# Performance work log

Hardware: AMD Instinct MI355X
Metric: run time of the kernel (lower is better)

The kernel has to match this reference:

```python
import jax, jax.numpy as jnp
import numpy as np

NUM_HEADS = 32


def setup_inputs() -> dict:
    key = jax.random.key(0)
    ks = jax.random.split(key, 6)
    B, S, E = 1, 2048, 2560
    return {
        "hidden_states": jax.random.normal(ks[0], (B, S, E), dtype=jnp.float32),
        "attention_mask": jnp.zeros((B, 1, 1, S), dtype=jnp.float32),
        "position_bias": jax.random.normal(ks[1], (NUM_HEADS, S, S), dtype=jnp.float32),
        "c_attn_w": jax.random.normal(ks[2], (E, 3 * E), dtype=jnp.float32) * 0.02,
        "c_attn_b": jax.random.normal(ks[3], (3 * E,), dtype=jnp.float32) * 0.02,
        "c_proj_w": jax.random.normal(ks[4], (E, E), dtype=jnp.float32) * 0.02,
        "c_proj_b": jax.random.normal(ks[5], (E,), dtype=jnp.float32) * 0.02,
    }


def reference(hidden_states, attention_mask, position_bias, c_attn_w, c_attn_b, c_proj_w, c_proj_b):
    B, S, E = hidden_states.shape
    H = NUM_HEADS
    D = E // H  # head_dim = 80

    # Fused QKV projection (GPT2-style Conv1D: x @ W + b)
    qkv = hidden_states @ c_attn_w + c_attn_b            # [B, S, 3E]
    q, k, v = jnp.split(qkv, 3, axis=-1)

    def split_heads(t):
        return t.reshape(B, S, H, D).transpose(0, 2, 1, 3)  # [B, H, S, D]

    q, k, v = split_heads(q), split_heads(k), split_heads(v)

    # muP scaling: attn_scale_power=1.0 -> divide by head_dim (not sqrt)
    scores = jnp.einsum("bhqd,bhkd->bhqk", q, k) / jnp.asarray(D, q.dtype)
    scores = scores + attention_mask                     # additive mask [B,1,1,S]
    scores = scores + position_bias[None]                # ALiBi bias [1,H,S,S]

    attn = jax.nn.softmax(scores, axis=-1)               # dropout p=0 -> identity
    out = jnp.einsum("bhqk,bhkd->bhqd", attn, v)         # [B, H, S, D]
    out = out.transpose(0, 2, 1, 3).reshape(B, S, E)     # merge heads

    out = out @ c_proj_w + c_proj_b                      # output projection
    return out
```

## Files before the change

kernel.cpp:

```cpp
#include <hip/hip_runtime.h>
#include <stdint.h>

#define S_LEN 2048
#define EMB   2560
#define NH    32
#define HD    80
#define DP    96

typedef __bf16 bf16x8 __attribute__((ext_vector_type(8)));
typedef float  f32x4  __attribute__((ext_vector_type(4)));

__device__ __forceinline__ ushort f2bf(float x) {
    union { float f; uint32_t u; } v; v.f = x;
    return (ushort)((v.u + 0x7FFFu + ((v.u >> 16) & 1u)) >> 16);
}

__device__ __forceinline__ bf16x8 ldg8(const ushort* p) {
    return *reinterpret_cast<const bf16x8*>(p);
}

__device__ __forceinline__ void gload_lds16(const void* g, void* l) {
    __builtin_amdgcn_global_load_lds((__attribute__((address_space(1))) void*)g,
                                     (__attribute__((address_space(3))) void*)l,
                                     16, 0, 0);
}

__global__ void cvt_f32_bf16(const float* __restrict__ in, ushort* __restrict__ out, int n4) {
    int i = blockIdx.x * blockDim.x + threadIdx.x;
    if (i >= n4) return;
    float4 v = reinterpret_cast<const float4*>(in)[i];
    ushort4 r;
    r.x = f2bf(v.x); r.y = f2bf(v.y); r.z = f2bf(v.z); r.w = f2bf(v.w);
    reinterpret_cast<ushort4*>(out)[i] = r;
}

__global__ void pad_zero(ushort* __restrict__ Qb, ushort* __restrict__ Kb) {
    int i   = blockIdx.x * blockDim.x + threadIdx.x;
    int row = i & 65535;
    ushort* base = ((i >> 16) ? Kb : Qb) + (size_t)row * DP + HD;
    uint4 z = {0, 0, 0, 0};
    *reinterpret_cast<uint4*>(base)     = z;
    *reinterpret_cast<uint4*>(base + 8) = z;
}

__global__ void transpose_cvt(const float* __restrict__ in, ushort* __restrict__ out, int R, int C) {
    __shared__ float tile[32][33];
    const int bx = blockIdx.x << 5;
    const int by = blockIdx.y << 5;
    const int tx = threadIdx.x, ty = threadIdx.y;
#pragma unroll
    for (int i = 0; i < 4; ++i)
        tile[ty + 8 * i][tx] = in[(size_t)(by + ty + 8 * i) * C + bx + tx];
    __syncthreads();
#pragma unroll
    for (int i = 0; i < 4; ++i)
        out[(size_t)(bx + ty + 8 * i) * R + by + tx] = f2bf(tile[tx][ty + 8 * i]);
}

#define MF(a, b, c) __builtin_amdgcn_mfma_f32_16x16x32_bf16((a), (b), (c), 0, 0, 0)

#define STAGE(kt2, j) do {                                                          \
    char* _d = Lds + ((kt2) % 3) * 49152 + ldsW[(j)];                               \
    if ((j) < 2) gload_lds16(aG + (size_t)(kt2) * 128 + srcA[(j)], _d);             \
    else         gload_lds16(bG + (size_t)(kt2) * 128 + srcB[(j) - 2], _d);         \
} while (0)

#define LDA(mi, kk) (*(const bf16x8*)(sbase + ((wr * 64 + (mi) * 16 + lo) * 128 +   \
                      ((((kk) * 64) + hi * 16) ^ ((lo & 7) << 4)))))
#define LDB(ni, kk) (*(const bf16x8*)(sbase + 16384 +                               \
                      ((wc * 64 + (ni) * 16 + lo) * 128 +                           \
                      ((((kk) * 64) + hi * 16) ^ ((lo & 7) << 4)))))

__global__ __launch_bounds__(512)
void gemm8p_qkv(const ushort* __restrict__ A, const ushort* __restrict__ BT,
                const float* __restrict__ bvec,
                ushort* __restrict__ Qo, ushort* __restrict__ Ko, ushort* __restrict__ Vo)
{
    __shared__ char Lds[3 * 49152];

    const int NT  = 40;
    const int nbn = 30;
    const int bid = blockIdx.x;
    const int wg  = (bid & 7) * 60 + (bid >> 3);
    const int bm  = wg / nbn, bn = wg - bm * nbn;

    const int tid = threadIdx.x, w = tid >> 6, lane = tid & 63;
    const int lo  = lane & 15, hi = lane >> 4;
    const int wr  = w >> 2, wc = w & 3;

    const char* aG = (const char*)(A  + (size_t)bm * 128 * 2560);
    const char* bG = (const char*)(BT + (size_t)bn * 256 * 2560);

    int srcA[2], srcB[4], ldsW[6];
#pragma unroll
    for (int j = 0; j < 6; ++j) {
        int Lb = j * 8192 + w * 1024 + lane * 16;
        ldsW[j] = j * 8192 + w * 1024;
        int y = Lb & 127;
        if (j < 2) {
            int r = Lb >> 7;
            srcA[j] = r * 5120 + (y ^ ((r & 7) << 4));
        } else {
            int r = (Lb - 16384) >> 7;
            srcB[j - 2] = r * 5120 + (y ^ ((r & 7) << 4));
        }
    }

    f32x4  acc[4][4] = {};
    bf16x8 Afr[2][2], Bfr[4][2];

#pragma unroll
    for (int j = 0; j < 6; ++j) STAGE(0, j);
#pragma unroll
    for (int j = 0; j < 6; ++j) STAGE(1, j);

#pragma unroll 1
    for (int t = 0; t < NT; ++t) {
        const char* sbase = Lds + (t % 3) * 49152;
        const int  t2 = t + 2;
        const bool pf = (t2 < NT);

        if (t < NT - 1) asm volatile("s_waitcnt vmcnt(6)" ::: "memory");
        else            asm volatile("s_waitcnt vmcnt(0)" ::: "memory");
        __builtin_amdgcn_s_barrier();

        Afr[0][0] = LDA(0, 0); Afr[0][1] = LDA(0, 1);
        Afr[1][0] = LDA(1, 0); Afr[1][1] = LDA(1, 1);
        Bfr[0][0] = LDB(0, 0); Bfr[0][1] = LDB(0, 1);
        Bfr[1][0] = LDB(1, 0); Bfr[1][1] = LDB(1, 1);
        if (pf) { STAGE(t2, 0); STAGE(t2, 1); }
        __builtin_amdgcn_s_barrier();
        asm volatile("s_waitcnt lgkmcnt(0)" ::: "memory");
        __builtin_amdgcn_sched_barrier(0);
        __builtin_amdgcn_s_setprio(1);
        acc[0][0] = MF(Afr[0][0], Bfr[0][0], acc[0][0]); acc[0][0] = MF(Afr[0][1], Bfr[0][1], acc[0][0]);
        acc[0][1] = MF(Afr[0][0], Bfr[1][0], acc[0][1]); acc[0][1] = MF(Afr[0][1], Bfr[1][1], acc[0][1]);
        acc[1][0] = MF(Afr[1][0], Bfr[0][0], acc[1][0]); acc[1][0] = MF(Afr[1][1], Bfr[0][1], acc[1][0]);
        acc[1][1] = MF(Afr[1][0], Bfr[1][0], acc[1][1]); acc[1][1] = MF(Afr[1][1], Bfr[1][1], acc[1][1]);
        __builtin_amdgcn_s_setprio(0);

        Bfr[2][0] = LDB(2, 0); Bfr[2][1] = LDB(2, 1);
        Bfr[3][0] = LDB(3, 0); Bfr[3][1] = LDB(3, 1);
        if (pf) { STAGE(t2, 2); STAGE(t2, 3); }
        __builtin_amdgcn_s_barrier();
        asm volatile("s_waitcnt lgkmcnt(0)" ::: "memory");
        __builtin_amdgcn_sched_barrier(0);
        __builtin_amdgcn_s_setprio(1);
        acc[0][2] = MF(Afr[0][0], Bfr[2][0], acc[0][2]); acc[0][2] = MF(Afr[0][1], Bfr[2][1], acc[0][2]);
        acc[0][3] = MF(Afr[0][0], Bfr[3][0], acc[0][3]); acc[0][3] = MF(Afr[0][1], Bfr[3][1], acc[0][3]);
        acc[1][2] = MF(Afr[1][0], Bfr[2][0], acc[1][2]); acc[1][2] = MF(Afr[1][1], Bfr[2][1], acc[1][2]);
        acc[1][3] = MF(Afr[1][0], Bfr[3][0], acc[1][3]); acc[1][3] = MF(Afr[1][1], Bfr[3][1], acc[1][3]);
        __builtin_amdgcn_s_setprio(0);

        Afr[0][0] = LDA(2, 0); Afr[0][1] = LDA(2, 1);
        Afr[1][0] = LDA(3, 0); Afr[1][1] = LDA(3, 1);
        if (pf) STAGE(t2, 4);
        __builtin_amdgcn_s_barrier();
        asm volatile("s_waitcnt lgkmcnt(0)" ::: "memory");
        __builtin_amdgcn_sched_barrier(0);
        __builtin_amdgcn_s_setprio(1);
        acc[2][2] = MF(Afr[0][0], Bfr[2][0], acc[2][2]); acc[2][2] = MF(Afr[0][1], Bfr[2][1], acc[2][2]);
        acc[2][3] = MF(Afr[0][0], Bfr[3][0], acc[2][3]); acc[2][3] = MF(Afr[0][1], Bfr[3][1], acc[2][3]);
        acc[3][2] = MF(Afr[1][0], Bfr[2][0], acc[3][2]); acc[3][2] = MF(Afr[1][1], Bfr[2][1], acc[3][2]);
        acc[3][3] = MF(Afr[1][0], Bfr[3][0], acc[3][3]); acc[3][3] = MF(Afr[1][1], Bfr[3][1], acc[3][3]);
        __builtin_amdgcn_s_setprio(0);

        if (pf) STAGE(t2, 5);
        __builtin_amdgcn_s_barrier();
        __builtin_amdgcn_s_setprio(1);
        acc[2][0] = MF(Afr[0][0], Bfr[0][0], acc[2][0]); acc[2][0] = MF(Afr[0][1], Bfr[0][1], acc[2][0]);
        acc[2][1] = MF(Afr[0][0], Bfr[1][0], acc[2][1]); acc[2][1] = MF(Afr[0][1], Bfr[1][1], acc[2][1]);
        acc[3][0] = MF(Afr[1][0], Bfr[0][0], acc[3][0]); acc[3][0] = MF(Afr[1][1], Bfr[0][1], acc[3][0]);
        acc[3][1] = MF(Afr[1][0], Bfr[1][0], acc[3][1]); acc[3][1] = MF(Afr[1][1], Bfr[1][1], acc[3][1]);
        __builtin_amdgcn_s_setprio(0);
    }

    const int gr_base = bm * 128 + wr * 64;
    const int gc_base = bn * 256 + wc * 64;
#pragma unroll
    for (int m = 0; m < 4; ++m) {
        int gr0 = gr_base + (m << 4) + (hi << 2);
#pragma unroll
        for (int n = 0; n < 4; ++n) {
            int gc = gc_base + (n << 4) + lo;
            float bv = bvec[gc];
            int sec = gc / EMB;
            int rr  = gc - sec * EMB;
            int h   = rr / HD;
            int d   = rr - h * HD;
            if (sec == 2) {
                ushort4 pk;
                pk.x = f2bf(acc[m][n][0] + bv);
                pk.y = f2bf(acc[m][n][1] + bv);
                pk.z = f2bf(acc[m][n][2] + bv);
                pk.w = f2bf(acc[m][n][3] + bv);
                *reinterpret_cast<ushort4*>(Vo + ((size_t)h * HD + d) * S_LEN + gr0) = pk;
            } else {
#pragma unroll
                for (int j = 0; j < 4; ++j) {
                    float vv = acc[m][n][j] + bv;
                    int s = gr0 + j;
                    if (sec == 0) Qo[((size_t)h * S_LEN + s) * DP + d] = f2bf(vv * (1.0f / 80.0f));
                    else          Ko[((size_t)h * S_LEN + s) * DP + d] = f2bf(vv);
                }
            }
        }
    }
}

template <int EPI>
__global__ __launch_bounds__(256)
void gemm_bt(const ushort* __restrict__ A, const ushort* __restrict__ BT,
             int M, int N, int Kd, const float* __restrict__ bvec,
             ushort* __restrict__ Qo, ushort* __restrict__ Ko, ushort* __restrict__ Vo,
             float* __restrict__ Co)
{
    __shared__ ushort As[128 * 64];
    __shared__ ushort Bs[128 * 64];

    const int nbn = N >> 7;
    const int nwg = gridDim.x;
    const int cpx = nwg >> 3;
    const int bid = blockIdx.x;
    const int wg  = (bid & 7) * cpx + (bid >> 3);
    const int bm  = wg / nbn;
    const int bn  = wg - bm * nbn;

    const int tid  = threadIdx.x;
    const int w    = tid >> 6, lane = tid & 63;
    const int lo   = lane & 15, hi = lane >> 4;
    const int wr   = w >> 1, wc = w & 1;

    const int srow  = tid >> 3;
    const int sbyte = (tid & 7) << 4;

    f32x4 acc[4][4] = {};

    const char* aG = (const char*)(A  + (size_t)bm * 128 * Kd);
    const char* bG = (const char*)(BT + (size_t)bn * 128 * Kd);
    const size_t rowBytes = (size_t)Kd * 2;

    for (int k0 = 0; k0 < Kd; k0 += 64) {
        __syncthreads();
#pragma unroll
        for (int is = 0; is < 4; ++is) {
            int r  = (is << 5) + srow;
            int sw = sbyte ^ ((r & 7) << 4);
            const char* ga = aG + (size_t)r * rowBytes + (size_t)k0 * 2 + sw;
            const char* gb = bG + (size_t)r * rowBytes + (size_t)k0 * 2 + sw;
            char* la = (char*)As + (is << 12) + (w << 10);
            char* lb = (char*)Bs + (is << 12) + (w << 10);
            gload_lds16(ga, la);
            gload_lds16(gb, lb);
        }
        asm volatile("s_waitcnt vmcnt(0)" ::: "memory");
        __syncthreads();
#pragma unroll
        for (int kk = 0; kk < 2; ++kk) {
            bf16x8 af[4], bf[4];
#pragma unroll
            for (int m = 0; m < 4; ++m) {
                int r   = (wr << 6) + (m << 4) + lo;
                int off = (r << 7) + ((((kk << 6) + (hi << 4))) ^ ((r & 7) << 4));
                af[m] = *(const bf16x8*)((const char*)As + off);
            }
#pragma unroll
            for (int n = 0; n < 4; ++n) {
                int r   = (wc << 6) + (n << 4) + lo;
                int off = (r << 7) + ((((kk << 6) + (hi << 4))) ^ ((r & 7) << 4));
                bf[n] = *(const bf16x8*)((const char*)Bs + off);
            }
#pragma unroll
            for (int m = 0; m < 4; ++m)
#pragma unroll
                for (int n = 0; n < 4; ++n)
                    acc[m][n] = __builtin_amdgcn_mfma_f32_16x16x32_bf16(af[m], bf[n], acc[m][n], 0, 0, 0);
        }
    }

    const int gr_base = bm * 128 + (wr << 6);
    const int gc_base = bn * 128 + (wc << 6);
#pragma unroll
    for (int m = 0; m < 4; ++m) {
        int gr0 = gr_base + (m << 4) + (hi << 2);
#pragma unroll
        for (int n = 0; n < 4; ++n) {
            int gc = gc_base + (n << 4) + lo;
            float bv = bvec[gc];
#pragma unroll
            for (int j = 0; j < 4; ++j)
                Co[(size_t)(gr0 + j) * N + gc] = acc[m][n][j] + bv;
        }
    }
}

__global__ __launch_bounds__(512, 4)
void attn_fwd(const ushort* __restrict__ Q, const ushort* __restrict__ K,
              const ushort* __restrict__ VT, const float* __restrict__ bias,
              const float* __restrict__ mask, ushort* __restrict__ ctx)
{
    __shared__ ushort Ks[2][64 * 96];
    __shared__ ushort Vs[2][80 * 64];
    __shared__ ushort P[8][16][72];

    const int bid = blockIdx.x;
    const int l_  = (bid & 7) * 64 + (bid >> 3);
    const int h   = l_ >> 4;
    const int qb  = (l_ & 15) << 7;
    const int tid = threadIdx.x;
    const int w   = tid >> 6, lane = tid & 63;
    const int lo  = lane & 15, hi = lane >> 4;
    const int qrow = qb + (w << 4);

    const ushort* qp = Q + ((size_t)(h * S_LEN + qrow + lo)) * DP + hi * 8;
    bf16x8 qf0 = ldg8(qp), qf1 = ldg8(qp + 32), qf2 = ldg8(qp + 64);

    const char*  kg = (const char*)(K + (size_t)h * S_LEN * DP);
    const char*  vg = (const char*)(VT + (size_t)h * HD * S_LEN);
    const float* bb = bias + (size_t)(h * S_LEN + qrow + hi * 4) * S_LEN + lo;

    int offK0, offK1;
    {
        int b0 = (w << 10) + lane * 16;
        int r0 = b0 / 192, y0 = b0 - r0 * 192;
        offK0 = r0 * 192 + (y0 ^ ((y0 < 128 ? (r0 & 7) : (r0 & 3)) << 4));
        int b1 = ((w + 8) << 10) + lane * 16;
        int r1 = b1 / 192, y1 = b1 - r1 * 192;
        offK1 = r1 * 192 + (y1 ^ ((y1 < 128 ? (r1 & 7) : (r1 & 3)) << 4));
    }

    f32x4 o[5] = {};
    float l_p[4] = {0.f, 0.f, 0.f, 0.f};
    float m_r[4] = {-1e30f, -1e30f, -1e30f, -1e30f};
    float bc[4][4], bn[4][4], mn_[4];

    auto stage_k = [&](int buf, int kt) {
        const char* src = kg + (size_t)kt * 192;
        gload_lds16(src + offK0, (char*)Ks[buf] + (w << 10));
        if (w < 4)
            gload_lds16(src + offK1, (char*)Ks[buf] + ((w + 8) << 10));
    };
    auto stage_v = [&](int buf, int kt) {
        int r0 = (w << 3) + (lane >> 3);
        int s0 = ((lane & 7) << 4) ^ ((r0 & 7) << 4);
        gload_lds16(vg + (size_t)r0 * (S_LEN * 2) + (size_t)kt * 2 + s0,
                    (char*)Vs[buf] + (w << 10));
        if (w < 2) {
            int r1 = ((w + 8) << 3) + (lane >> 3);
            int s1 = ((lane & 7) << 4) ^ ((r1 & 7) << 4);
            gload_lds16(vg + (size_t)r1 * (S_LEN * 2) + (size_t)kt * 2 + s1,
                        (char*)Vs[buf] + ((w + 8) << 10));
        }
    };
    auto bload = [&](int kt) {
#pragma unroll
        for (int n = 0; n < 4; ++n) {
            mn_[n] = mask[kt + n * 16 + lo];
#pragma unroll
            for (int j = 0; j < 4; ++j)
                bn[n][j] = __builtin_nontemporal_load(bb + (size_t)j * S_LEN + kt + n * 16);
        }
    };
    auto rotate = [&]() {
#pragma unroll
        for (int n = 0; n < 4; ++n)
#pragma unroll
            for (int j = 0; j < 4; ++j)
                bc[n][j] = bn[n][j] + mn_[n];
    };

    stage_k(0, 0); stage_v(0, 0); bload(0); rotate();
    __syncthreads();

#pragma unroll 1
    for (int t = 0; t < 32; ++t) {
        const int kt = t << 6;
        const int cb = t & 1;
        if (t < 31) { stage_k(cb ^ 1, kt + 64); stage_v(cb ^ 1, kt + 64); bload(kt + 64); }

        const char* tb = (const char*)Ks[cb];
        f32x4 sc[4] = {};
        __builtin_amdgcn_s_setprio(1);
#pragma unroll
        for (int n = 0; n < 4; ++n) {
            const int r  = (n << 4) + lo;
            const char* rp = tb + r * 192;
            const int s7 = (r & 7) << 4, s3 = (r & 3) << 4;
            sc[n] = __builtin_amdgcn_mfma_f32_16x16x32_bf16(qf0, *(const bf16x8*)(rp + ((hi * 16) ^ s7)),        sc[n], 0, 0, 0);
            sc[n] = __builtin_amdgcn_mfma_f32_16x16x32_bf16(qf1, *(const bf16x8*)(rp + ((64 + hi * 16) ^ s7)),   sc[n], 0, 0, 0);
            sc[n] = __builtin_amdgcn_mfma_f32_16x16x32_bf16(qf2, *(const bf16x8*)(rp + ((128 + hi * 16) ^ s3)),  sc[n], 0, 0, 0);
        }
        __builtin_amdgcn_s_setprio(0);

#pragma unroll
        for (int n = 0; n < 4; ++n)
#pragma unroll
            for (int j = 0; j < 4; ++j)
                sc[n][j] += bc[n][j];

        float tm[4];
#pragma unroll
        for (int j = 0; j < 4; ++j)
            tm[j] = fmaxf(fmaxf(sc[0][j], sc[1][j]), fmaxf(sc[2][j], sc[3][j]));
#pragma unroll
        for (int off = 1; off <= 8; off <<= 1)
#pragma unroll
            for (int j = 0; j < 4; ++j)
                tm[j] = fmaxf(tm[j], __shfl_xor(tm[j], off, 64));

        float al[4];
#pragma unroll
        for (int j = 0; j < 4; ++j) {
            float mnew = fmaxf(m_r[j], tm[j]);
            al[j] = __builtin_amdgcn_exp2f((m_r[j] - mnew) * 1.44269504f);
            m_r[j] = mnew;
            l_p[j] *= al[j];
        }
#pragma unroll
        for (int dn = 0; dn < 5; ++dn)
#pragma unroll
            for (int j = 0; j < 4; ++j)
                o[dn][j] *= al[j];
#pragma unroll
        for (int n = 0; n < 4; ++n)
#pragma unroll
            for (int j = 0; j < 4; ++j) {
                float p = __builtin_amdgcn_exp2f((sc[n][j] - m_r[j]) * 1.44269504f);
                l_p[j] += p;
                P[w][hi * 4 + j][n * 16 + lo] = f2bf(p);
            }
        asm volatile("s_waitcnt lgkmcnt(0)" ::: "memory");
        __builtin_amdgcn_sched_barrier(0);
        bf16x8 pf0 = ldg8(&P[w][lo][hi * 8]);
        bf16x8 pf1 = ldg8(&P[w][lo][32 + hi * 8]);

        const char* vb_ = (const char*)Vs[cb];
        __builtin_amdgcn_s_setprio(1);
#pragma unroll
        for (int dn = 0; dn < 5; ++dn) {
            const int rv = (dn << 4) + lo;
            const char* vp = vb_ + (rv << 7);
            const int sv = (rv & 7) << 4;
            o[dn] = __builtin_amdgcn_mfma_f32_16x16x32_bf16(pf0, *(const bf16x8*)(vp + ((hi * 16) ^ sv)),      o[dn], 0, 0, 0);
            o[dn] = __builtin_amdgcn_mfma_f32_16x16x32_bf16(pf1, *(const bf16x8*)(vp + ((64 + hi * 16) ^ sv)), o[dn], 0, 0, 0);
        }
        __builtin_amdgcn_s_setprio(0);

        rotate();
        __syncthreads();
    }

    float inv[4];
#pragma unroll
    for (int j = 0; j < 4; ++j) {
        float t = l_p[j];
        t += __shfl_xor(t, 1, 64); t += __shfl_xor(t, 2, 64);
        t += __shfl_xor(t, 4, 64); t += __shfl_xor(t, 8, 64);
        inv[j] = 1.0f / t;
    }
    ushort* cp = ctx + (size_t)(qrow + hi * 4) * EMB + h * HD + lo;
#pragma unroll
    for (int dn = 0; dn < 5; ++dn)
#pragma unroll
        for (int j = 0; j < 4; ++j)
            cp[(size_t)j * EMB + dn * 16] = f2bf(o[dn][j] * inv[j]);
}

extern "C" void kernel_launch(void* const* d_in, const int* in_sizes, int n_in,
                              void* d_out, int out_size, void* d_ws, size_t ws_size,
                              hipStream_t stream)
{
    const float* hs     = (const float*)d_in[0];
    const float* mask   = (const float*)d_in[1];
    const float* pbias  = (const float*)d_in[2];
    const float* attn_w = (const float*)d_in[3];
    const float* attn_b = (const float*)d_in[4];
    const float* proj_w = (const float*)d_in[5];
    const float* proj_b = (const float*)d_in[6];
    float* outp = (float*)d_out;

    char* ws = (char*)d_ws;
    ushort* hsB    = (ushort*)(ws);
    ushort* attnWT = (ushort*)(ws + 10485760ull);
    ushort* Qb     = (ushort*)(ws + 49807360ull);
    ushort* Kb     = (ushort*)(ws + 62390272ull);
    ushort* VTb    = (ushort*)(ws + 74973184ull);
    ushort* ctx    = hsB;
    ushort* projWT = attnWT;

    cvt_f32_bf16<<<5120, 256, 0, stream>>>(hs, hsB, 1310720);
    transpose_cvt<<<dim3(7680 / 32, 2560 / 32), dim3(32, 8), 0, stream>>>(attn_w, attnWT, 2560, 7680);
    pad_zero<<<512, 256, 0, stream>>>(Qb, Kb);

    gemm8p_qkv<<<480, 512, 0, stream>>>(hsB, attnWT, attn_b, Qb, Kb, VTb);

    attn_fwd<<<512, 512, 0, stream>>>(Qb, Kb, VTb, pbias, mask, ctx);

    transpose_cvt<<<dim3(2560 / 32, 2560 / 32), dim3(32, 8), 0, stream>>>(proj_w, projWT, 2560, 2560);

    gemm_bt<1><<<320, 256, 0, stream>>>(ctx, projWT, 2048, 2560, 2560, proj_b,
                                        nullptr, nullptr, nullptr, outp);
}
```

Measured before the change: 343.6 us.

## Stage position bias tiles into LDS via async global-to-LDS loads in attention

The attention kernel now copies each 128x64 fp32 tile of the position bias into a double-buffered, swizzled LDS buffer with global_load_lds, instead of having each thread issue strided nontemporal register loads. The tile is then read back from LDS and the mask is added inline. This is meant to make the dominant bias stream coalesced and asynchronous and to free the registers used for prefetching. In exchange it adds 64KB of LDS per block and lowers the occupancy hint from 4 to 2 blocks per CU. Unused parameters are also removed from gemm_bt.

```diff
diff --git a/kernel.cpp b/kernel.cpp
--- a/kernel.cpp
+++ b/kernel.cpp
@@ -212,7 +212,6 @@
 __global__ __launch_bounds__(256)
 void gemm_bt(const ushort* __restrict__ A, const ushort* __restrict__ BT,
              int M, int N, int Kd, const float* __restrict__ bvec,
-             ushort* __restrict__ Qo, ushort* __restrict__ Ko, ushort* __restrict__ Vo,
              float* __restrict__ Co)
 {
     __shared__ ushort As[128 * 64];
@@ -294,13 +293,14 @@
     }
 }
 
-__global__ __launch_bounds__(512, 4)
+__global__ __launch_bounds__(512, 2)
 void attn_fwd(const ushort* __restrict__ Q, const ushort* __restrict__ K,
               const ushort* __restrict__ VT, const float* __restrict__ bias,
               const float* __restrict__ mask, ushort* __restrict__ ctx)
 {
     __shared__ ushort Ks[2][64 * 96];
     __shared__ ushort Vs[2][80 * 64];
+    __shared__ float  Bs[2][128 * 64];
     __shared__ ushort P[8][16][72];
 
     const int bid = blockIdx.x;
@@ -315,9 +315,9 @@
     const ushort* qp = Q + ((size_t)(h * S_LEN + qrow + lo)) * DP + hi * 8;
     bf16x8 qf0 = ldg8(qp), qf1 = ldg8(qp + 32), qf2 = ldg8(qp + 64);
 
-    const char*  kg = (const char*)(K + (size_t)h * S_LEN * DP);
-    const char*  vg = (const char*)(VT + (size_t)h * HD * S_LEN);
-    const float* bb = bias + (size_t)(h * S_LEN + qrow + hi * 4) * S_LEN + lo;
+    const char* kg = (const char*)(K + (size_t)h * S_LEN * DP);
+    const char* vg = (const char*)(VT + (size_t)h * HD * S_LEN);
+    const char* bg = (const char*)(bias + ((size_t)h * S_LEN + qb) * S_LEN);
 
     int offK0, offK1;
     {
@@ -328,11 +328,20 @@
         int r1 = b1 / 192, y1 = b1 - r1 * 192;
         offK1 = r1 * 192 + (y1 ^ ((y1 < 128 ? (r1 & 7) : (r1 & 3)) << 4));
     }
+    int offB[4], dstB[4];
+    {
+#pragma unroll
+        for (int q = 0; q < 4; ++q) {
+            int b = q * 8192 + tid * 16;
+            int r = b >> 8, y = b & 255;
+            offB[q] = r * 8192 + (y ^ (((r >> 2) & 3) << 5));
+            dstB[q] = q * 8192 + (w << 10);
+        }
+    }
 
     f32x4 o[5] = {};
     float l_p[4] = {0.f, 0.f, 0.f, 0.f};
     float m_r[4] = {-1e30f, -1e30f, -1e30f, -1e30f};
-    float bc[4][4], bn[4][4], mn_[4];
 
     auto stage_k = [&](int buf, int kt) {
         const char* src = kg + (size_t)kt * 192;
@@ -352,31 +361,21 @@
                         (char*)Vs[buf] + ((w + 8) << 10));
         }
     };
-    auto bload = [&](int kt) {
-#pragma unroll
-        for (int n = 0; n < 4; ++n) {
-            mn_[n] = mask[kt + n * 16 + lo];
-#pragma unroll
-            for (int j = 0; j < 4; ++j)
-                bn[n][j] = __builtin_nontemporal_load(bb + (size_t)j * S_LEN + kt + n * 16);
-        }
+    auto stage_b = [&](int buf, int kt) {
+        const char* src = bg + (size_t)kt * 4;
+#pragma unroll
+        for (int q = 0; q < 4; ++q)
+            gload_lds16(src + offB[q], (char*)Bs[buf] + dstB[q]);
     };
-    auto rotate = [&]() {
-#pragma unroll
-        for (int n = 0; n < 4; ++n)
-#pragma unroll
-            for (int j = 0; j < 4; ++j)
-                bc[n][j] = bn[n][j] + mn_[n];
-    };
-
-    stage_k(0, 0); stage_v(0, 0); bload(0); rotate();
+
+    stage_k(0, 0); stage_v(0, 0); stage_b(0, 0);
     __syncthreads();
 
 #pragma unroll 1
     for (int t = 0; t < 32; ++t) {
         const int kt = t << 6;
         const int cb = t & 1;
-        if (t < 31) { stage_k(cb ^ 1, kt + 64); stage_v(cb ^ 1, kt + 64); bload(kt + 64); }
+        if (t < 31) { stage_k(cb ^ 1, kt + 64); stage_v(cb ^ 1, kt + 64); stage_b(cb ^ 1, kt + 64); }
 
         const char* tb = (const char*)Ks[cb];
         f32x4 sc[4] = {};
@@ -392,11 +391,17 @@
         }
         __builtin_amdgcn_s_setprio(0);
 
-#pragma unroll
-        for (int n = 0; n < 4; ++n)
-#pragma unroll
-            for (int j = 0; j < 4; ++j)
-                sc[n][j] += bc[n][j];
+        {
+            const char* bsb = (const char*)Bs[cb] + ((w << 4) + (hi << 2)) * 256;
+            const int sw = hi << 5;
+#pragma unroll
+            for (int n = 0; n < 4; ++n) {
+                float mk = mask[kt + n * 16 + lo];
+#pragma unroll
+                for (int j = 0; j < 4; ++j)
+                    sc[n][j] += *(const float*)(bsb + j * 256 + ((((n << 4) + lo) << 2) ^ sw)) + mk;
+            }
+        }
 
         float tm[4];
 #pragma unroll
@@ -446,7 +451,6 @@
         }
         __builtin_amdgcn_s_setprio(0);
 
-        rotate();
         __syncthreads();
     }
 
@@ -498,6 +502,5 @@
 
     transpose_cvt<<<dim3(2560 / 32, 2560 / 32), dim3(32, 8), 0, stream>>>(proj_w, projWT, 2560, 2560);
 
-    gemm_bt<1><<<320, 256, 0, stream>>>(ctx, projWT, 2048, 2560, 2560, proj_b,
-                                        nullptr, nullptr, nullptr, outp);
-}
+    gemm_bt<1><<<320, 256, 0, stream>>>(ctx, projWT, 2048, 2560, 2560, proj_b, outp);
+}
```

After: 393.0 us. 14.4% more time.

## Restructure attention loop with merged K/V staging and two-deep bias prefetch

Applied to the files above, without the earlier changes.

The attention kernel merges the K and V LDS buffers into one double-buffered region. Every wave now issues exactly three async global-to-LDS loads per tile, using precomputed source pointers. The ALiBi bias and mask loads are prefetched two tiles ahead into ping-pong register sets, and the loop is unrolled by two. The full __syncthreads is replaced by a counted vmcnt wait plus s_barrier, so in-flight bias loads can overlap the barrier. This is meant to hide bias-load latency behind compute, at the cost of more registers and fragile hand-tuned wait counts.

```diff
diff --git a/kernel.cpp b/kernel.cpp
--- a/kernel.cpp
+++ b/kernel.cpp
@@ -212,7 +212,6 @@
 __global__ __launch_bounds__(256)
 void gemm_bt(const ushort* __restrict__ A, const ushort* __restrict__ BT,
              int M, int N, int Kd, const float* __restrict__ bvec,
-             ushort* __restrict__ Qo, ushort* __restrict__ Ko, ushort* __restrict__ Vo,
              float* __restrict__ Co)
 {
     __shared__ ushort As[128 * 64];
@@ -299,8 +298,7 @@
               const ushort* __restrict__ VT, const float* __restrict__ bias,
               const float* __restrict__ mask, ushort* __restrict__ ctx)
 {
-    __shared__ ushort Ks[2][64 * 96];
-    __shared__ ushort Vs[2][80 * 64];
+    __shared__ char   KV[2][22528];
     __shared__ ushort P[8][16][72];
 
     const int bid = blockIdx.x;
@@ -319,76 +317,59 @@
     const char*  vg = (const char*)(VT + (size_t)h * HD * S_LEN);
     const float* bb = bias + (size_t)(h * S_LEN + qrow + hi * 4) * S_LEN + lo;
 
-    int offK0, offK1;
-    {
-        int b0 = (w << 10) + lane * 16;
-        int r0 = b0 / 192, y0 = b0 - r0 * 192;
-        offK0 = r0 * 192 + (y0 ^ ((y0 < 128 ? (r0 & 7) : (r0 & 3)) << 4));
-        int b1 = ((w + 8) << 10) + lane * 16;
-        int r1 = b1 / 192, y1 = b1 - r1 * 192;
-        offK1 = r1 * 192 + (y1 ^ ((y1 < 128 ? (r1 & 7) : (r1 & 3)) << 4));
+    const char* sSrc[3]; int sStr[3], sDst[3];
+#pragma unroll
+    for (int s = 0; s < 3; ++s) {
+        int c = w + 8 * s;
+        if (c < 12) {
+            int b = c * 1024 + lane * 16;
+            int r = b / 192, y = b - r * 192;
+            int y2 = y ^ ((y < 128 ? (r & 7) : (r & 3)) << 4);
+            sSrc[s] = kg + r * 192 + y2;
+            sStr[s] = 64 * 192;
+            sDst[s] = c * 1024;
+        } else {
+            int cv = (c < 22) ? c - 12 : c - 22;
+            int rv = cv * 8 + (lane >> 3);
+            int s0 = ((lane & 7) << 4) ^ ((rv & 7) << 4);
+            sSrc[s] = vg + (size_t)rv * (S_LEN * 2) + s0;
+            sStr[s] = 128;
+            sDst[s] = 12288 + cv * 1024;
+        }
     }
 
     f32x4 o[5] = {};
     float l_p[4] = {0.f, 0.f, 0.f, 0.f};
     float m_r[4] = {-1e30f, -1e30f, -1e30f, -1e30f};
-    float bc[4][4], bn[4][4], mn_[4];
-
-    auto stage_k = [&](int buf, int kt) {
-        const char* src = kg + (size_t)kt * 192;
-        gload_lds16(src + offK0, (char*)Ks[buf] + (w << 10));
-        if (w < 4)
-            gload_lds16(src + offK1, (char*)Ks[buf] + ((w + 8) << 10));
+    float bkA[4][4], mkA[4], bkB[4][4], mkB[4];
+
+    auto stage = [&](char* dstBuf, int tt) {
+#pragma unroll
+        for (int s = 0; s < 3; ++s)
+            gload_lds16(sSrc[s] + (size_t)tt * sStr[s], dstBuf + sDst[s]);
     };
-    auto stage_v = [&](int buf, int kt) {
-        int r0 = (w << 3) + (lane >> 3);
-        int s0 = ((lane & 7) << 4) ^ ((r0 & 7) << 4);
-        gload_lds16(vg + (size_t)r0 * (S_LEN * 2) + (size_t)kt * 2 + s0,
-                    (char*)Vs[buf] + (w << 10));
-        if (w < 2) {
-            int r1 = ((w + 8) << 3) + (lane >> 3);
-            int s1 = ((lane & 7) << 4) ^ ((r1 & 7) << 4);
-            gload_lds16(vg + (size_t)r1 * (S_LEN * 2) + (size_t)kt * 2 + s1,
-                        (char*)Vs[buf] + ((w + 8) << 10));
+    auto bload = [&](int tt, float (&bk)[4][4], float (&mk)[4]) {
+        const int kt2 = tt << 6;
+#pragma unroll
+        for (int n = 0; n < 4; ++n) {
+            mk[n] = mask[kt2 + n * 16 + lo];
+#pragma unroll
+            for (int j = 0; j < 4; ++j)
+                bk[n][j] = __builtin_nontemporal_load(bb + (size_t)j * S_LEN + kt2 + n * 16);
         }
     };
-    auto bload = [&](int kt) {
-#pragma unroll
-        for (int n = 0; n < 4; ++n) {
-            mn_[n] = mask[kt + n * 16 + lo];
-#pragma unroll
-            for (int j = 0; j < 4; ++j)
-                bn[n][j] = __builtin_nontemporal_load(bb + (size_t)j * S_LEN + kt + n * 16);
-        }
-    };
-    auto rotate = [&]() {
-#pragma unroll
-        for (int n = 0; n < 4; ++n)
-#pragma unroll
-            for (int j = 0; j < 4; ++j)
-                bc[n][j] = bn[n][j] + mn_[n];
-    };
-
-    stage_k(0, 0); stage_v(0, 0); bload(0); rotate();
-    __syncthreads();
-
-#pragma unroll 1
-    for (int t = 0; t < 32; ++t) {
-        const int kt = t << 6;
-        const int cb = t & 1;
-        if (t < 31) { stage_k(cb ^ 1, kt + 64); stage_v(cb ^ 1, kt + 64); bload(kt + 64); }
-
-        const char* tb = (const char*)Ks[cb];
+
+    auto iterf = [&](int t, char* buf, char* obuf, float (&bk)[4][4], float (&mk)[4]) {
         f32x4 sc[4] = {};
         __builtin_amdgcn_s_setprio(1);
 #pragma unroll
         for (int n = 0; n < 4; ++n) {
             const int r  = (n << 4) + lo;
-            const char* rp = tb + r * 192;
+            const char* rp = buf + r * 192;
             const int s7 = (r & 7) << 4, s3 = (r & 3) << 4;
-            sc[n] = __builtin_amdgcn_mfma_f32_16x16x32_bf16(qf0, *(const bf16x8*)(rp + ((hi * 16) ^ s7)),        sc[n], 0, 0, 0);
-            sc[n] = __builtin_amdgcn_mfma_f32_16x16x32_bf16(qf1, *(const bf16x8*)(rp + ((64 + hi * 16) ^ s7)),   sc[n], 0, 0, 0);
-            sc[n] = __builtin_amdgcn_mfma_f32_16x16x32_bf16(qf2, *(const bf16x8*)(rp + ((128 + hi * 16) ^ s3)),  sc[n], 0, 0, 0);
+            sc[n] = __builtin_amdgcn_mfma_f32_16x16x32_bf16(qf0, *(const bf16x8*)(rp + ((hi * 16) ^ s7)),       sc[n], 0, 0, 0);
+            sc[n] = __builtin_amdgcn_mfma_f32_16x16x32_bf16(qf1, *(const bf16x8*)(rp + ((64 + hi * 16) ^ s7)),  sc[n], 0, 0, 0);
+            sc[n] = __builtin_amdgcn_mfma_f32_16x16x32_bf16(qf2, *(const bf16x8*)(rp + ((128 + hi * 16) ^ s3)), sc[n], 0, 0, 0);
         }
         __builtin_amdgcn_s_setprio(0);
 
@@ -396,7 +377,12 @@
         for (int n = 0; n < 4; ++n)
 #pragma unroll
             for (int j = 0; j < 4; ++j)
-                sc[n][j] += bc[n][j];
+                sc[n][j] += bk[n][j] + mk[n];
+
+        if (t + 1 < 32) stage(obuf, t + 1);
+        __builtin_amdgcn_sched_barrier(0);
+        if (t + 2 < 32) bload(t + 2, bk, mk);
+        __builtin_amdgcn_sched_barrier(0);
 
         float tm[4];
 #pragma unroll
@@ -434,7 +420,7 @@
         bf16x8 pf0 = ldg8(&P[w][lo][hi * 8]);
         bf16x8 pf1 = ldg8(&P[w][lo][32 + hi * 8]);
 
-        const char* vb_ = (const char*)Vs[cb];
+        const char* vb_ = buf + 12288;
         __builtin_amdgcn_s_setprio(1);
 #pragma unroll
         for (int dn = 0; dn < 5; ++dn) {
@@ -446,17 +432,31 @@
         }
         __builtin_amdgcn_s_setprio(0);
 
-        rotate();
-        __syncthreads();
+        if (t + 2 < 32)      asm volatile("s_waitcnt vmcnt(20)" ::: "memory");
+        else if (t + 1 < 32) asm volatile("s_waitcnt vmcnt(0)" ::: "memory");
+        if (t + 1 < 32) __builtin_amdgcn_s_barrier();
+    };
+
+    stage(KV[0], 0);
+    __builtin_amdgcn_sched_barrier(0);
+    bload(0, bkA, mkA);
+    bload(1, bkB, mkB);
+    asm volatile("s_waitcnt vmcnt(20)" ::: "memory");
+    __builtin_amdgcn_s_barrier();
+
+#pragma unroll 1
+    for (int t = 0; t < 32; t += 2) {
+        iterf(t,     KV[0], KV[1], bkA, mkA);
+        iterf(t + 1, KV[1], KV[0], bkB, mkB);
     }
 
     float inv[4];
 #pragma unroll
     for (int j = 0; j < 4; ++j) {
-        float t = l_p[j];
-        t += __shfl_xor(t, 1, 64); t += __shfl_xor(t, 2, 64);
-        t += __shfl_xor(t, 4, 64); t += __shfl_xor(t, 8, 64);
-        inv[j] = 1.0f / t;
+        float tt = l_p[j];
+        tt += __shfl_xor(tt, 1, 64); tt += __shfl_xor(tt, 2, 64);
+        tt += __shfl_xor(tt, 4, 64); tt += __shfl_xor(tt, 8, 64);
+        inv[j] = 1.0f / tt;
     }
     ushort* cp = ctx + (size_t)(qrow + hi * 4) * EMB + h * HD + lo;
 #pragma unroll
@@ -498,6 +498,5 @@
 
     transpose_cvt<<<dim3(2560 / 32, 2560 / 32), dim3(32, 8), 0, stream>>>(proj_w, projWT, 2560, 2560);
 
-    gemm_bt<1><<<320, 256, 0, stream>>>(ctx, projWT, 2048, 2560, 2560, proj_b,
-                                        nullptr, nullptr, nullptr, outp);
-}
+    gemm_bt<1><<<320, 256, 0, stream>>>(ctx, projWT, 2048, 2560, 2560, proj_b, outp);
+}
```

Measured after the change: 544.8 us. 1.59x slower.
